# Kernel tuning notes

Measured on AMD Instinct MI355X. Metric: run time of the kernel, lower is better.

Reference implementation:

```python
import jax, jax.numpy as jnp
import numpy as np

N = 65536      # total nodes
B = 128        # graphs per batch
NPG = N // B   # nodes per graph (equal-size graphs)
IN = 128       # in_channels
H = 128        # hidden_channels
E = 1048576    # spatial edges
K = 8          # kNN neighbors
L = 3          # num_layers
EPS = 1e-5     # GraphNorm eps
SLOPE = 0.01   # leaky_relu default negative_slope


def setup_inputs() -> dict:
    key = jax.random.key(0)
    ks = jax.random.split(key, 16)
    x = jax.random.normal(ks[0], (N, IN), jnp.float32)
    edge_index = jax.random.randint(ks[1], (2, E), 0, N, dtype=jnp.int32)
    batch = jnp.repeat(jnp.arange(B, dtype=jnp.int32), NPG)
    s = 0.05
    inp = {
        'x': x, 'edge_index': edge_index, 'batch': batch,
        'emb_w': jax.random.normal(ks[2], (IN, H), jnp.float32) * s,
        'emb_b': jax.random.normal(ks[3], (H,), jnp.float32) * s,
        'conv_w': jax.random.normal(ks[4], (L - 1, H, H), jnp.float32) * s,
        'conv_b': jax.random.normal(ks[5], (L - 1, H), jnp.float32) * s,
        'fconv_w': jax.random.normal(ks[6], (L - 1, H, H), jnp.float32) * s,
        'fconv_b': jax.random.normal(ks[7], (L - 1, H), jnp.float32) * s,
        'norm_w': 1.0 + jax.random.normal(ks[8], (L - 1, H), jnp.float32) * s,
        'norm_b': jax.random.normal(ks[9], (L - 1, H), jnp.float32) * s,
        'norm_ms': 1.0 + jax.random.normal(ks[10], (L - 1, H), jnp.float32) * s,
        'fnorm_w': 1.0 + jax.random.normal(ks[11], (L - 1, H), jnp.float32) * s,
        'fnorm_b': jax.random.normal(ks[12], (L - 1, H), jnp.float32) * s,
        'fnorm_ms': 1.0 + jax.random.normal(ks[13], (L - 1, H), jnp.float32) * s,
    }
    return inp


def _segment_mean(v, seg, num):
    s = jax.ops.segment_sum(v, seg, num_segments=num)
    c = jax.ops.segment_sum(jnp.ones((v.shape[0], 1), v.dtype), seg, num_segments=num)
    return s / jnp.maximum(c, 1.0)


def _gcn_conv(h, src, dst, W, b):
    # GCNConv: h @ W, add self-loops, symmetric normalization, scatter-add.
    hw = h @ W
    deg = jax.ops.segment_sum(jnp.ones(src.shape[0], hw.dtype), dst, num_segments=N) + 1.0
    dinv = jax.lax.rsqrt(deg)
    msgs = (dinv[src] * dinv[dst])[:, None] * hw[src]
    agg = jnp.zeros_like(hw).at[dst].add(msgs)
    agg = agg + (dinv * dinv)[:, None] * hw  # self-loop contribution
    return agg + b


def _graph_norm(v, batch, w, bsh, ms):
    mean = _segment_mean(v, batch, B)                  # [B,H]
    out = v - mean[batch] * ms
    var = _segment_mean(out * out, batch, B)
    std = jnp.sqrt(var + EPS)
    return w * out / std[batch] + bsh


def _knn_graph_cosine(h):
    # per-graph cosine kNN (loop=False); equal-size graphs -> blocked [B,n,n] sim
    hb = h.reshape(B, NPG, H)
    nrm = jnp.linalg.norm(hb, axis=-1, keepdims=True)
    hn = hb / jnp.maximum(nrm, 1e-12)
    sim = jnp.einsum('bnd,bmd->bnm', hn, hn)
    sim = sim - 2.0 * jnp.eye(NPG, dtype=sim.dtype)    # exclude self-loops
    _, idx = jax.lax.top_k(sim, K)                     # [B,NPG,K] in-graph ids
    offs = (jnp.arange(B, dtype=idx.dtype) * NPG)[:, None, None]
    src = (idx + offs).reshape(-1).astype(jnp.int32)   # neighbors (sources)
    dst = jnp.repeat(jnp.arange(N, dtype=jnp.int32), K)
    return src, dst


def reference(x, edge_index, batch, emb_w, emb_b, conv_w, conv_b, fconv_w, fconv_b,
              norm_w, norm_b, norm_ms, fnorm_w, fnorm_b, fnorm_ms):
    h = x @ emb_w + emb_b
    fsrc, fdst = _knn_graph_cosine(h)
    src, dst = edge_index[0], edge_index[1]
    all_h = []
    for i in range(L - 1):
        h1 = _gcn_conv(h, src, dst, conv_w[i], conv_b[i])
        h1 = _graph_norm(h1, batch, norm_w[i], norm_b[i], norm_ms[i])
        h1 = jax.nn.leaky_relu(h1, SLOPE)              # dropout is identity (eval)
        f = _gcn_conv(h1, fsrc, fdst, fconv_w[i], fconv_b[i])
        f = _graph_norm(f, batch, fnorm_w[i], fnorm_b[i], fnorm_ms[i])
        f = jax.nn.leaky_relu(f, SLOPE)
        h = (h1 + f) * 0.5
        all_h.append(h)
    # faithful to original: indexes all_x[i-1] for i in range(num_layers)
    gf = jnp.zeros((B, H), h.dtype)
    for i in range(L):
        gf = gf + _segment_mean(all_h[i - 1], batch, B)
    return gf
```

## Files before the change

### kernel.cpp

```cpp
#include <hip/hip_runtime.h>

typedef unsigned short u16;
typedef unsigned int   u32;
typedef unsigned char  u8;
typedef __bf16 bf16x8 __attribute__((ext_vector_type(8)));
typedef unsigned short us8 __attribute__((ext_vector_type(8)));
typedef float f32x4 __attribute__((ext_vector_type(4)));

#define NN 65536
#define EE 1048576
#define NPGC 512
#define BGR 128
#define ESL 8
#define EMAX 32
#define FP8S 32.0f
#define FP8SI (1.0f/32.0f)

__device__ inline float bf2f(u16 b){ u32 u=((u32)b)<<16; float f; __builtin_memcpy(&f,&u,4); return f; }
__device__ inline u16 f2bf(float f){ u32 u; __builtin_memcpy(&u,&f,4); u32 r=(u+0x7FFFu+((u>>16)&1u))>>16; return (u16)r; }
__device__ inline u8 f2fp8(float f){
  int p = __builtin_amdgcn_cvt_pk_fp8_f32(f, f, 0, false);
  return (u8)(p & 0xFF);
}

struct PTab { const void* src[9]; int off[9]; };
__global__ __launch_bounds__(256) void prep_params(const float* __restrict__ emb_w,
    const float* __restrict__ conv_w, const float* __restrict__ fconv_w, u16* __restrict__ pwt,
    PTab tab, u16* __restrict__ pw)
{
  int i = blockIdx.x*256 + threadIdx.x;
  if (i < 5*16384) {
    int m = i >> 14, j = i & 16383;
    int n = j >> 7, k = j & 127;
    const float* src = (m == 0) ? emb_w : (m <= 2) ? conv_w + (m-1)*16384 : fconv_w + (m-3)*16384;
    pwt[i] = f2bf(src[k*128 + n]);
  } else {
    int s = i - 5*16384;
    if (s < 2176) {
      int t = 0;
      #pragma unroll
      for (int k = 1; k < 9; k++) if (s >= tab.off[k]) t = k;
      pw[s] = f2bf(((const float*)tab.src[t])[s - tab.off[t]]);
    }
  }
}

__global__ __launch_bounds__(256) void gemm_emb_bt(const float* __restrict__ X,
    const u16* __restrict__ BtE, const u16* __restrict__ bias, const u16* __restrict__ BtC,
    const float* __restrict__ dinvp, u16* __restrict__ Ch, float* __restrict__ rinv,
    u8* __restrict__ Chw)
{
  __shared__ __align__(16) u16 hs[64][136];
  const int tid = threadIdx.x;
  const int wave = tid >> 6, lane = tid & 63, q = lane >> 4, l15 = lane & 15;
  const long arow = (long)blockIdx.x*64 + wave*16 + l15;
  const float* Ap = X + arow*128;
  f32x4 acc[8] = {};
  #pragma unroll
  for (int ks = 0; ks < 4; ks++) {
    const int k0 = ks*32 + q*8;
    float4 u0 = *reinterpret_cast<const float4*>(Ap + k0);
    float4 u1 = *reinterpret_cast<const float4*>(Ap + k0 + 4);
    us8 a;
    a[0]=f2bf(u0.x); a[1]=f2bf(u0.y); a[2]=f2bf(u0.z); a[3]=f2bf(u0.w);
    a[4]=f2bf(u1.x); a[5]=f2bf(u1.y); a[6]=f2bf(u1.z); a[7]=f2bf(u1.w);
    bf16x8 af = __builtin_bit_cast(bf16x8, a);
    #pragma unroll
    for (int nt = 0; nt < 8; nt++) {
      bf16x8 bf = __builtin_bit_cast(bf16x8,
          *reinterpret_cast<const us8*>(BtE + (nt*16 + l15)*128 + k0));
      acc[nt] = __builtin_amdgcn_mfma_f32_16x16x32_bf16(af, bf, acc[nt], 0, 0, 0);
    }
  }
  const long orow0 = (long)blockIdx.x*64 + wave*16 + q*4;
  float bvt[8];
  #pragma unroll
  for (int nt = 0; nt < 8; nt++) bvt[nt] = bf2f(bias[nt*16 + l15]);
  #pragma unroll
  for (int r = 0; r < 4; r++) {
    float ss = 0.f;
    const int lrow = wave*16 + q*4 + r;
    #pragma unroll
    for (int nt = 0; nt < 8; nt++) {
      float hv = acc[nt][r] + bvt[nt];
      u16 hb = f2bf(hv);
      Ch[(orow0 + r)*128 + nt*16 + l15] = hb;
      hs[lrow][nt*16 + l15] = hb;
      ss += hv*hv;
    }
    #pragma unroll
    for (int m = 1; m < 16; m <<= 1) ss += __shfl_xor(ss, m, 64);
    if (l15 == 0) rinv[orow0 + r] = 1.0f / fmaxf(sqrtf(ss), 1e-12f);
  }
  __syncthreads();
  f32x4 acc2[8] = {};
  #pragma unroll
  for (int ks = 0; ks < 4; ks++) {
    const int k0 = ks*32 + q*8;
    bf16x8 af = __builtin_bit_cast(bf16x8,
        *reinterpret_cast<const us8*>(&hs[wave*16 + l15][k0]));
    #pragma unroll
    for (int nt = 0; nt < 8; nt++) {
      bf16x8 bf = __builtin_bit_cast(bf16x8,
          *reinterpret_cast<const us8*>(BtC + (nt*16 + l15)*128 + k0));
      acc2[nt] = __builtin_amdgcn_mfma_f32_16x16x32_bf16(af, bf, acc2[nt], 0, 0, 0);
    }
  }
  float scl[4];
  #pragma unroll
  for (int r = 0; r < 4; r++) scl[r] = dinvp[orow0 + r] * FP8S;
  #pragma unroll
  for (int nt = 0; nt < 8; nt++) {
    int col = nt*16 + l15;
    #pragma unroll
    for (int r = 0; r < 4; r++)
      Chw[(orow0 + r)*128 + col] = f2fp8(acc2[nt][r] * scl[r]);
  }
}

__global__ __launch_bounds__(256) void gemm_norm(const u16* __restrict__ h1raw,
    const u16* __restrict__ Bt, const float* __restrict__ ssum, const float* __restrict__ ssq,
    const u16* __restrict__ gw, const u16* __restrict__ gb, const u16* __restrict__ gms,
    u16* __restrict__ h1norm, u16* __restrict__ C)
{
  __shared__ float As[128], Bs[128];
  const int tid = threadIdx.x;
  const int gidx = blockIdx.x >> 3;
  if (tid < 128) {
    float mean = ssum[gidx*128 + tid] * (1.0f/512.0f);
    float e2   = ssq [gidx*128 + tid] * (1.0f/512.0f);
    float sub  = mean * bf2f(gms[tid]);
    float var  = e2 - 2.0f*sub*mean + sub*sub;
    float istd = rsqrtf(var + 1e-5f);
    float A = istd * bf2f(gw[tid]);
    As[tid] = A;
    Bs[tid] = bf2f(gb[tid]) - sub*A;
  }
  __syncthreads();
  const int wave = tid >> 6, lane = tid & 63, q = lane >> 4, l15 = lane & 15;
  const long arow = (long)blockIdx.x*64 + wave*16 + l15;
  const u16* Ap = h1raw + arow*128;
  f32x4 acc[8] = {};
  #pragma unroll
  for (int ks = 0; ks < 4; ks++) {
    const int k0 = ks*32 + q*8;
    us8 raw = *reinterpret_cast<const us8*>(Ap + k0);
    us8 af;
    #pragma unroll
    for (int j = 0; j < 8; j++) {
      float o = As[k0+j] * bf2f(raw[j]) + Bs[k0+j];
      o = (o >= 0.f) ? o : 0.01f * o;
      af[j] = f2bf(o);
    }
    *reinterpret_cast<us8*>(h1norm + arow*128 + k0) = af;
    bf16x8 afv = __builtin_bit_cast(bf16x8, af);
    #pragma unroll
    for (int nt = 0; nt < 8; nt++) {
      bf16x8 bf = __builtin_bit_cast(bf16x8,
          *reinterpret_cast<const us8*>(Bt + (nt*16 + l15)*128 + k0));
      acc[nt] = __builtin_amdgcn_mfma_f32_16x16x32_bf16(afv, bf, acc[nt], 0, 0, 0);
    }
  }
  const long orow0 = (long)blockIdx.x*64 + wave*16 + q*4;
  #pragma unroll
  for (int nt = 0; nt < 8; nt++) {
    int col = nt*16 + l15;
    #pragma unroll
    for (int r = 0; r < 4; r++)
      C[(orow0 + r)*128 + col] = f2bf(acc[nt][r]);
  }
}

__global__ __launch_bounds__(256) void gn_apply_gemm(const u16* __restrict__ fraw,
    const u16* __restrict__ h1n, const u16* __restrict__ Bt,
    const float* __restrict__ ssum, const float* __restrict__ ssq,
    const u16* __restrict__ gw, const u16* __restrict__ gb, const u16* __restrict__ gms,
    const float* __restrict__ dinvp, float* __restrict__ gf, u8* __restrict__ C)
{
  __shared__ float As[128], Bs[128];
  __shared__ float gpart[4][128];
  const int tid = threadIdx.x;
  const int gidx = blockIdx.x >> 3;
  if (tid < 128) {
    float mean = ssum[gidx*128 + tid] * (1.0f/512.0f);
    float e2   = ssq [gidx*128 + tid] * (1.0f/512.0f);
    float sub  = mean * bf2f(gms[tid]);
    float var  = e2 - 2.0f*sub*mean + sub*sub;
    float istd = rsqrtf(var + 1e-5f);
    float A = istd * bf2f(gw[tid]);
    As[tid] = A;
    Bs[tid] = bf2f(gb[tid]) - sub*A;
  }
  __syncthreads();
  const int wave = tid >> 6, lane = tid & 63, q = lane >> 4, l15 = lane & 15;
  const long arow = (long)blockIdx.x*64 + wave*16 + l15;
  const u16* Fp = fraw + arow*128;
  const u16* Hp = h1n  + arow*128;
  f32x4 acc[8] = {};
  float hv[4][8];
  #pragma unroll
  for (int ks = 0; ks < 4; ks++) {
    const int k0 = ks*32 + q*8;
    us8 fr = *reinterpret_cast<const us8*>(Fp + k0);
    us8 hr = *reinterpret_cast<const us8*>(Hp + k0);
    us8 af;
    #pragma unroll
    for (int j = 0; j < 8; j++) {
      float o = As[k0+j] * bf2f(fr[j]) + Bs[k0+j];
      o = (o >= 0.f) ? o : 0.01f * o;
      float h = 0.5f * (bf2f(hr[j]) + o);
      hv[ks][j] = h;
      af[j] = f2bf(h);
    }
    bf16x8 afv = __builtin_bit_cast(bf16x8, af);
    #pragma unroll
    for (int nt = 0; nt < 8; nt++) {
      bf16x8 bf = __builtin_bit_cast(bf16x8,
          *reinterpret_cast<const us8*>(Bt + (nt*16 + l15)*128 + k0));
      acc[nt] = __builtin_amdgcn_mfma_f32_16x16x32_bf16(afv, bf, acc[nt], 0, 0, 0);
    }
  }
  const long orow0 = (long)blockIdx.x*64 + wave*16 + q*4;
  float scl[4];
  #pragma unroll
  for (int r = 0; r < 4; r++) scl[r] = dinvp[orow0 + r] * FP8S;
  #pragma unroll
  for (int nt = 0; nt < 8; nt++) {
    int col = nt*16 + l15;
    #pragma unroll
    for (int r = 0; r < 4; r++)
      C[(orow0 + r)*128 + col] = f2fp8(acc[nt][r] * scl[r]);
  }
  #pragma unroll
  for (int ks = 0; ks < 4; ks++) {
    #pragma unroll
    for (int j = 0; j < 8; j++) {
      float v = hv[ks][j];
      v += __shfl_xor(v, 1, 64);
      v += __shfl_xor(v, 2, 64);
      v += __shfl_xor(v, 4, 64);
      v += __shfl_xor(v, 8, 64);
      if (l15 == 0) gpart[wave][ks*32 + q*8 + j] = v;
    }
  }
  __syncthreads();
  if (tid < 128) {
    float s = gpart[0][tid] + gpart[1][tid] + gpart[2][tid] + gpart[3][tid];
    atomicAdd(&gf[gidx*128 + tid], s * (1.0f/512.0f));
  }
}

__global__ void fill_ell(const int* __restrict__ srcp, const int* __restrict__ dstp,
    int* __restrict__ pos2, u16* __restrict__ ell){
  int base = (blockIdx.x*256 + threadIdx.x) * 4;
  int cls = blockIdx.x & 7;
  int4 dv = *reinterpret_cast<const int4*>(dstp + base);
  int4 sv = *reinterpret_cast<const int4*>(srcp + base);
  #pragma unroll
  for (int t = 0; t < 4; t++) {
    int d = ((&dv.x)[t]) & (NN-1);
    int p = atomicAdd(&pos2[cls*NN + d], 1);
    if (p < ESL) ell[((size_t)cls*NN + d)*ESL + p] = (u16)(((&sv.x)[t]) & (NN-1));
  }
}

__global__ __launch_bounds__(256) void repack_ell(const int* __restrict__ pos2,
    const u16* __restrict__ ell_cls, u16* __restrict__ elln, int* __restrict__ deg,
    float* __restrict__ dinv)
{
  int n = blockIdx.x*256 + threadIdx.x;
  u16* dst = elln + ((size_t)n << 5);
  int w = 0, tot = 0;
  #pragma unroll
  for (int c = 0; c < 8; c++) {
    int cnt = pos2[c*NN + n];
    tot += cnt;
    cnt = min(cnt, ESL);
    us8 iv = *reinterpret_cast<const us8*>(ell_cls + ((size_t)c*NN + n)*ESL);
    for (int t = 0; t < cnt; t++) { if (w < EMAX) dst[w] = iv[t]; w++; }
  }
  deg[n] = min(w, EMAX);
  dinv[n] = rsqrtf((float)tot + 1.0f);
}

__device__ inline u32 mkkey(float v, u32 col){
  u32 b; __builtin_memcpy(&b, &v, 4);
  b ^= (u32)(((int)b >> 31)) | 0x80000000u;
  return (b & 0xFFFFFE00u) | col;
}
#define TOP8_INS(tv, key) { \
  tv[0] = max(tv[0], (key)); \
  u32 lo_, hi_; \
  lo_ = min(tv[0],tv[1]); hi_ = max(tv[0],tv[1]); tv[0]=lo_; tv[1]=hi_; \
  lo_ = min(tv[1],tv[2]); hi_ = max(tv[1],tv[2]); tv[1]=lo_; tv[2]=hi_; \
  lo_ = min(tv[2],tv[3]); hi_ = max(tv[2],tv[3]); tv[2]=lo_; tv[3]=hi_; \
  lo_ = min(tv[3],tv[4]); hi_ = max(tv[3],tv[4]); tv[3]=lo_; tv[4]=hi_; \
  lo_ = min(tv[4],tv[5]); hi_ = max(tv[4],tv[5]); tv[4]=lo_; tv[5]=hi_; \
  lo_ = min(tv[5],tv[6]); hi_ = max(tv[5],tv[6]); tv[5]=lo_; tv[6]=hi_; \
  lo_ = min(tv[6],tv[7]); hi_ = max(tv[6],tv[7]); tv[6]=lo_; tv[7]=hi_; }

__global__ __launch_bounds__(256, 4) void knn_topk(const u16* __restrict__ h,
    const float* __restrict__ rinv, int* __restrict__ fsrc)
{
  __shared__ __align__(16) u16 Bb[64*136];
  __shared__ __align__(16) u32 simb[64*68];
  __shared__ float rb[64];
  const int tid = threadIdx.x;
  const int g = blockIdx.x & 127, tile = blockIdx.x >> 7;
  const int gbase = g * NPGC;
  const int abase = gbase + tile * 64;
  const int wave = tid >> 6, lane = tid & 63, q = lane >> 4, l15 = lane & 15;

  us8 afr[4];
  #pragma unroll
  for (int ks = 0; ks < 4; ks++)
    afr[ks] = *reinterpret_cast<const us8*>(h + (size_t)(abase + wave*16 + l15)*128 + ks*32 + q*8);

  const int r0 = tid >> 4, c80 = (tid & 15) * 8;
  us8 breg[4];
  #pragma unroll
  for (int it = 0; it < 4; it++)
    breg[it] = *reinterpret_cast<const us8*>(h + (size_t)(gbase + r0 + it*16)*128 + c80);
  float rbreg = (tid < 64) ? rinv[gbase + tid] : 0.f;

  const int srow = tid >> 2, ssub = tid & 3;
  u32 tv[8];
  #pragma unroll
  for (int t = 0; t < 8; t++) tv[t] = 0u;

  for (int ch = 0; ch < 8; ch++) {
    #pragma unroll
    for (int it = 0; it < 4; it++)
      *reinterpret_cast<us8*>(&Bb[(r0 + it*16)*136 + c80]) = breg[it];
    if (tid < 64) rb[tid] = rbreg;
    __syncthreads();
    if (ch < 7) {
      #pragma unroll
      for (int it = 0; it < 4; it++)
        breg[it] = *reinterpret_cast<const us8*>(h + (size_t)(gbase + (ch+1)*64 + r0 + it*16)*128 + c80);
      if (tid < 64) rbreg = rinv[gbase + (ch+1)*64 + tid];
    }
    f32x4 acc[4] = {};
    #pragma unroll
    for (int ks = 0; ks < 4; ks++) {
      int k0 = ks*32 + q*8;
      bf16x8 af = __builtin_bit_cast(bf16x8, afr[ks]);
      #pragma unroll
      for (int ct = 0; ct < 4; ct++) {
        bf16x8 bf = __builtin_bit_cast(bf16x8, *reinterpret_cast<const us8*>(&Bb[(ct*16 + l15)*136 + k0]));
        acc[ct] = __builtin_amdgcn_mfma_f32_16x16x32_bf16(af, bf, acc[ct], 0, 0, 0);
      }
    }
    #pragma unroll
    for (int ct = 0; ct < 4; ct++) {
      int lc = ct*16 + l15;
      float rbv = rb[lc];
      #pragma unroll
      for (int r = 0; r < 4; r++) {
        int lr = wave*16 + q*4 + r;
        u32 key = mkkey(acc[ct][r] * rbv, (u32)(ch*64 + lc));
        if (tile*64 + lr == ch*64 + lc) key = 0u;
        simb[lr*68 + lc] = key;
      }
    }
    __syncthreads();
    const u32* sp = &simb[srow*68 + ssub*16];
    #pragma unroll
    for (int u = 0; u < 4; u++) {
      uint4 kv = *reinterpret_cast<const uint4*>(sp + 4*u);
      TOP8_INS(tv, kv.x); TOP8_INS(tv, kv.y); TOP8_INS(tv, kv.z); TOP8_INS(tv, kv.w);
    }
    __syncthreads();
  }
  u32* candk = simb;
  #pragma unroll
  for (int t = 0; t < 8; t++) candk[srow*33 + ssub*8 + t] = tv[t];
  __syncthreads();
  if (tid < 64) {
    u32 bv[8];
    #pragma unroll
    for (int t = 0; t < 8; t++) bv[t] = 0u;
    for (int t = 0; t < 32; t++) {
      u32 key = candk[tid*33 + t];
      TOP8_INS(bv, key);
    }
    size_t node = abase + tid;
    #pragma unroll
    for (int k2 = 0; k2 < 8; k2++) fsrc[node*8 + k2] = gbase + (int)(bv[k2] & 511u);
  }
}

__device__ inline void acc4(u32 vv, bool on, float& a0, float& a1, float& a2, float& a3){
  float c0 = __builtin_amdgcn_cvt_f32_fp8((int)vv, 0);
  float c1 = __builtin_amdgcn_cvt_f32_fp8((int)vv, 1);
  float c2 = __builtin_amdgcn_cvt_f32_fp8((int)vv, 2);
  float c3 = __builtin_amdgcn_cvt_f32_fp8((int)vv, 3);
  a0 += on ? c0 : 0.f; a1 += on ? c1 : 0.f;
  a2 += on ? c2 : 0.f; a3 += on ? c3 : 0.f;
}
__global__ __launch_bounds__(256) void agg_spatial(const u32* __restrict__ hw32,
    const u16* __restrict__ elln, const int* __restrict__ deg, const float* __restrict__ dinv,
    const u16* __restrict__ bias, u16* __restrict__ outp,
    float* __restrict__ ssum, float* __restrict__ ssq)
{
  __shared__ f32x4 sred[4][64], qred[4][64];
  const int g = blockIdx.x & 127, sub = blockIdx.x >> 7;
  const int wave = threadIdx.x >> 6, lane = threadIdx.x & 63;
  const int half = lane >> 5, cl = lane & 31;
  const int nbase = g*NPGC + sub*32 + wave*8;
  float bv[4];
  #pragma unroll
  for (int k = 0; k < 4; k++) bv[k] = bf2f(bias[4*cl + k]);
  float sa0=0,sa1=0,sa2=0,sa3=0, qa0=0,qa1=0,qa2=0,qa3=0;
  for (int t = 0; t < 4; t++) {
    const int node = nbase + 2*t + half;
    const u16* row = elln + ((size_t)node << 5);
    const int d = deg[node];
    const int dmax = max(d, __shfl_xor(d, 32, 64));
    const float dnS = dinv[node] * FP8SI;
    const u32 sv = hw32[(size_t)node*32 + cl];
    float a0=0,a1=0,a2=0,a3=0;
    if (dmax > 0) {
      us8 iv0 = *reinterpret_cast<const us8*>(row);
      us8 iv1 = *reinterpret_cast<const us8*>(row + 8);
      u32 v[16];
      #pragma unroll
      for (int u = 0; u < 8; u++) v[u] = hw32[(size_t)iv0[u]*32 + cl];
      const bool two = (dmax > 8);
      if (two) {
        #pragma unroll
        for (int u = 0; u < 8; u++) v[8+u] = hw32[(size_t)iv1[u]*32 + cl];
      }
      #pragma unroll
      for (int u = 0; u < 8; u++) acc4(v[u], u < d, a0, a1, a2, a3);
      if (two) {
        #pragma unroll
        for (int u = 0; u < 8; u++) acc4(v[8+u], 8+u < d, a0, a1, a2, a3);
      }
    }
    if (dmax > 16) {
      us8 iv2 = *reinterpret_cast<const us8*>(row + 16);
      us8 iv3 = *reinterpret_cast<const us8*>(row + 24);
      u32 v[16];
      #pragma unroll
      for (int u = 0; u < 8; u++) v[u] = hw32[(size_t)iv2[u]*32 + cl];
      const bool four = (dmax > 24);
      if (four) {
        #pragma unroll
        for (int u = 0; u < 8; u++) v[8+u] = hw32[(size_t)iv3[u]*32 + cl];
      }
      #pragma unroll
      for (int u = 0; u < 8; u++) acc4(v[u], 16+u < d, a0, a1, a2, a3);
      if (four) {
        #pragma unroll
        for (int u = 0; u < 8; u++) acc4(v[8+u], 24+u < d, a0, a1, a2, a3);
      }
    }
    acc4(sv, true, a0, a1, a2, a3);
    float r0 = dnS*a0 + bv[0], r1 = dnS*a1 + bv[1];
    float r2 = dnS*a2 + bv[2], r3 = dnS*a3 + bv[3];
    u32* op = reinterpret_cast<u32*>(outp) + (size_t)node*64 + 2*cl;
    op[0] = (u32)f2bf(r0) | ((u32)f2bf(r1) << 16);
    op[1] = (u32)f2bf(r2) | ((u32)f2bf(r3) << 16);
    sa0 += r0; sa1 += r1; sa2 += r2; sa3 += r3;
    qa0 += r0*r0; qa1 += r1*r1; qa2 += r2*r2; qa3 += r3*r3;
  }
  sred[wave][lane] = (f32x4){sa0, sa1, sa2, sa3};
  qred[wave][lane] = (f32x4){qa0, qa1, qa2, qa3};
  __syncthreads();
  const int tid = threadIdx.x;
  if (tid < 128) {
    const int ccl = tid >> 2, k = tid & 3;
    float s = 0.f, qq = 0.f;
    #pragma unroll
    for (int w = 0; w < 4; w++) {
      s  += sred[w][ccl][k] + sred[w][32+ccl][k];
      qq += qred[w][ccl][k] + qred[w][32+ccl][k];
    }
    atomicAdd(&ssum[g*128 + tid], s);
    atomicAdd(&ssq [g*128 + tid], qq);
  }
}

__global__ __launch_bounds__(256) void agg_knn(const u16* __restrict__ hw, const int* __restrict__ fsrc,
    const u16* __restrict__ bias, u16* __restrict__ outp,
    float* __restrict__ ssum, float* __restrict__ ssq)
{
  __shared__ float4 red[4][64];
  const int g = blockIdx.x & 127, sub = blockIdx.x >> 7;
  const int wave = threadIdx.x >> 6, lane = threadIdx.x & 63;
  const int nbase = g*NPGC + sub*32 + wave*8;
  const u32* hwp = reinterpret_cast<const u32*>(hw);
  const float bv0 = bf2f(bias[2*lane]), bv1 = bf2f(bias[2*lane+1]);
  const float c = 1.0f / 9.0f;
  float s0 = 0.f, s1 = 0.f, q0 = 0.f, q1 = 0.f;
  for (int t = 0; t < 8; t++) {
    const int node = nbase + t;
    const int* fr = fsrc + (long)node*8;
    u32 sv = hwp[(long)node*64 + lane];
    float a0 = bf2f((u16)sv), a1 = bf2f((u16)(sv>>16));
    #pragma unroll
    for (int k2 = 0; k2 < 8; k2++) {
      int s = fr[k2] & (NN-1);
      u32 v = hwp[(long)s*64 + lane];
      a0 += bf2f((u16)v); a1 += bf2f((u16)(v>>16));
    }
    float r0 = a0*c + bv0;
    float r1 = a1*c + bv1;
    reinterpret_cast<u32*>(outp)[(long)node*64 + lane] = (u32)f2bf(r0) | ((u32)f2bf(r1) << 16);
    s0 += r0; s1 += r1; q0 += r0*r0; q1 += r1*r1;
  }
  red[wave][lane] = make_float4(s0, s1, q0, q1);
  __syncthreads();
  if (wave == 0) {
    float4 a = red[0][lane];
    #pragma unroll
    for (int k = 1; k < 4; k++) {
      float4 b = red[k][lane];
      a.x += b.x; a.y += b.y; a.z += b.z; a.w += b.w;
    }
    atomicAdd(&ssum[g*128 + 2*lane],     a.x);
    atomicAdd(&ssum[g*128 + 2*lane + 1], a.y);
    atomicAdd(&ssq [g*128 + 2*lane],     a.z);
    atomicAdd(&ssq [g*128 + 2*lane + 1], a.w);
  }
}

__global__ __launch_bounds__(1024) void gn_final(const u16* __restrict__ v, const u16* __restrict__ h1n,
    const float* __restrict__ ssum, const float* __restrict__ ssq,
    const u16* __restrict__ gw, const u16* __restrict__ gb, const u16* __restrict__ gms,
    const float* __restrict__ gf, float* __restrict__ outf)
{
  __shared__ float red[1024];
  const int tid = threadIdx.x;
  const int g = blockIdx.x >> 1, half = blockIdx.x & 1;
  const int cl = tid & 63, c = half*64 + cl;
  const int rsub = tid >> 6;
  const long base = (long)g * NPGC * 128;
  float mean = ssum[g*128 + c] * (1.0f/512.0f);
  float e2   = ssq [g*128 + c] * (1.0f/512.0f);
  float sub  = mean * bf2f(gms[c]);
  float var  = e2 - 2.0f*sub*mean + sub*sub;
  float istd = rsqrtf(var + 1e-5f);
  float A = istd * bf2f(gw[c]);
  float B = bf2f(gb[c]) - sub*A;
  float gsum = 0.f;
  for (int r = rsub; r < NPGC; r += 16) {
    long idx = base + (long)r*128 + c;
    float o = A * bf2f(v[idx]) + B;
    o = (o >= 0.f) ? o : 0.01f * o;
    o = 0.5f * (bf2f(h1n[idx]) + o);
    gsum += o;
  }
  red[tid] = gsum; __syncthreads();
  if (tid < 64) {
    float t = 0.f;
    for (int k = 0; k < 16; k++) t += red[cl + k*64];
    int oi = g*128 + half*64 + tid;
    outf[oi] = gf[oi] + 2.0f * t * (1.0f/512.0f);
  }
}

extern "C" void kernel_launch(void* const* d_in, const int* in_sizes, int n_in,
                              void* d_out, int out_size, void* d_ws, size_t ws_size,
                              hipStream_t stream)
{
  const float* x  = (const float*)d_in[0];
  const int*   ei = (const int*)d_in[1];

  char* p = (char*)d_ws;
  auto alloc = [&](size_t b){ void* r = (void*)p; p += ((b + 255) & ~(size_t)255); return r; };
  u16*   h_bf   = (u16*)  alloc((size_t)NN*128*2);
  u16*   f_bf   = (u16*)  alloc((size_t)NN*128*2);
  u16*   h1_bf  = (u16*)  alloc((size_t)NN*128*2);
  int*   fsrc   = (int*)  alloc((size_t)NN*8*4);
  u16*   elln   = (u16*)  alloc((size_t)NN*32*2);
  int*   deg    = (int*)  alloc((size_t)NN*4);
  float* dinv   = (float*)alloc((size_t)NN*4);
  float* rinv   = (float*)alloc((size_t)NN*4);
  int*   pos2   = (int*)  alloc((size_t)8*NN*4);
  float* gf     = (float*)alloc((size_t)BGR*128*4);
  float* stats  = (float*)alloc((size_t)8*BGR*128*4);
  u16*   pw     = (u16*)  alloc((size_t)2176*2);
  u16*   pwt    = (u16*)  alloc((size_t)5*16384*2);
  char*  shared = (char*) alloc((size_t)NN*128*2);
  u16*   ell_cls = (u16*)shared;
  u16*   hw_bf   = (u16*)shared;
  u8*    hw_f8   = (u8*) shared;

  const int O_EMBB=0, O_CONVB=128, O_FCONVB=384, O_NW=640, O_NB=896, O_NMS=1152,
            O_FNW=1408, O_FNB=1664, O_FNMS=1920;
  PTab tab;
  const int srcidx[9] = {4,6,8,9,10,11,12,13,14};
  const int offs[9]   = {O_EMBB,O_CONVB,O_FCONVB,O_NW,O_NB,O_NMS,O_FNW,O_FNB,O_FNMS};
  for (int t = 0; t < 9; t++) { tab.src[t] = d_in[srcidx[t]]; tab.off[t] = offs[t]; }

  const int* srcp = ei;
  const int* dstp = ei + EE;

  (void)hipMemsetAsync(pos2, 0, (size_t)8*NN*4 + (size_t)BGR*128*4 + (size_t)8*BGR*128*4, stream);

  prep_params<<<329, 256, 0, stream>>>((const float*)d_in[3], (const float*)d_in[5],
                                       (const float*)d_in[7], pwt, tab, pw);
  fill_ell<<<1024, 256, 0, stream>>>(srcp, dstp, pos2, ell_cls);
  repack_ell<<<256, 256, 0, stream>>>(pos2, ell_cls, elln, deg, dinv);
  gemm_emb_bt<<<1024, 256, 0, stream>>>(x, pwt + 0, pw + O_EMBB, pwt + 1*16384, dinv,
                                        h_bf, rinv, hw_f8);
  knn_topk<<<1024, 256, 0, stream>>>(h_bf, rinv, fsrc);

  float* ssS0 = stats + 0*BGR*128; float* sqS0 = stats + 1*BGR*128;
  float* ssF0 = stats + 2*BGR*128; float* sqF0 = stats + 3*BGR*128;
  float* ssS1 = stats + 4*BGR*128; float* sqS1 = stats + 5*BGR*128;
  float* ssF1 = stats + 6*BGR*128; float* sqF1 = stats + 7*BGR*128;

  agg_spatial<<<2048, 256, 0, stream>>>((const u32*)hw_f8, elln, deg, dinv, pw + O_CONVB,
                                        h1_bf, ssS0, sqS0);
  gemm_norm<<<1024, 256, 0, stream>>>(h1_bf, pwt + 3*16384, ssS0, sqS0,
                                      pw + O_NW, pw + O_NB, pw + O_NMS,
                                      h_bf , hw_bf);
  agg_knn<<<2048, 256, 0, stream>>>(hw_bf, fsrc, pw + O_FCONVB, f_bf, ssF0, sqF0);
  gn_apply_gemm<<<1024, 256, 0, stream>>>(f_bf, h_bf, pwt + 2*16384, ssF0, sqF0,
                                          pw + O_FNW, pw + O_FNB, pw + O_FNMS,
                                          dinv, gf, hw_f8);
  agg_spatial<<<2048, 256, 0, stream>>>((const u32*)hw_f8, elln, deg, dinv, pw + O_CONVB + 128,
                                        h1_bf, ssS1, sqS1);
  gemm_norm<<<1024, 256, 0, stream>>>(h1_bf, pwt + 4*16384, ssS1, sqS1,
                                      pw + O_NW + 128, pw + O_NB + 128, pw + O_NMS + 128,
                                      h_bf , hw_bf);
  agg_knn<<<2048, 256, 0, stream>>>(hw_bf, fsrc, pw + O_FCONVB + 128, f_bf, ssF1, sqF1);
  gn_final<<<256, 1024, 0, stream>>>(f_bf, h_bf, ssF1, sqF1,
                                     pw + O_FNW + 128, pw + O_FNB + 128, pw + O_FNMS + 128,
                                     gf, (float*)d_out);
}
```

Baseline: 413.3 us.

## Build ELL adjacency directly with destination-partitioned atomics, drop repack kernel

Replaces the two-pass ELL build (eight per-class 8-slot buckets followed by a repack kernel) with a single pass. Each block reads a chunk of edges and only inserts those whose destination falls in its partition, writing straight into the 32-slot per-node list. Degree and the rsqrt normalisation are now recomputed on the fly from the position counter in the consumer kernels. The aim is to remove the repack launch and the deg/dinv arrays; in exchange every edge is read by eight blocks, and edges are now lost only past 32 per node rather than past 8 per class.

```diff
diff --git a/kernel.cpp b/kernel.cpp
--- a/kernel.cpp
+++ b/kernel.cpp
@@ -11,7 +11,6 @@
 #define EE 1048576
 #define NPGC 512
 #define BGR 128
-#define ESL 8
 #define EMAX 32
 #define FP8S 32.0f
 #define FP8SI (1.0f/32.0f)
@@ -45,9 +44,31 @@
   }
 }
 
+__global__ __launch_bounds__(256) void fill_ell(const int* __restrict__ srcp,
+    const int* __restrict__ dstp, int* __restrict__ pos, u16* __restrict__ elln)
+{
+  const int part  = blockIdx.x & 7;
+  const int chunk = blockIdx.x >> 3;
+  const int tid = threadIdx.x;
+  #pragma unroll
+  for (int v = 0; v < 8; v++) {
+    const int e = chunk*8192 + (v*256 + tid)*4;
+    int4 dv = *reinterpret_cast<const int4*>(dstp + e);
+    int4 sv = *reinterpret_cast<const int4*>(srcp + e);
+    #pragma unroll
+    for (int t = 0; t < 4; t++) {
+      int d = ((&dv.x)[t]) & (NN-1);
+      if ((d >> 13) == part) {
+        int p = atomicAdd(&pos[d], 1);
+        if (p < EMAX) elln[((size_t)d << 5) + p] = (u16)(((&sv.x)[t]) & (NN-1));
+      }
+    }
+  }
+}
+
 __global__ __launch_bounds__(256) void gemm_emb_bt(const float* __restrict__ X,
     const u16* __restrict__ BtE, const u16* __restrict__ bias, const u16* __restrict__ BtC,
-    const float* __restrict__ dinvp, u16* __restrict__ Ch, float* __restrict__ rinv,
+    const int* __restrict__ pos, u16* __restrict__ Ch, float* __restrict__ rinv,
     u8* __restrict__ Chw)
 {
   __shared__ __align__(16) u16 hs[64][136];
@@ -108,7 +129,7 @@
   }
   float scl[4];
   #pragma unroll
-  for (int r = 0; r < 4; r++) scl[r] = dinvp[orow0 + r] * FP8S;
+  for (int r = 0; r < 4; r++) scl[r] = rsqrtf((float)pos[orow0 + r] + 1.0f) * FP8S;
   #pragma unroll
   for (int nt = 0; nt < 8; nt++) {
     int col = nt*16 + l15;
@@ -175,7 +196,7 @@
     const u16* __restrict__ h1n, const u16* __restrict__ Bt,
     const float* __restrict__ ssum, const float* __restrict__ ssq,
     const u16* __restrict__ gw, const u16* __restrict__ gb, const u16* __restrict__ gms,
-    const float* __restrict__ dinvp, float* __restrict__ gf, u8* __restrict__ C)
+    const int* __restrict__ pos, float* __restrict__ gf, u8* __restrict__ C)
 {
   __shared__ float As[128], Bs[128];
   __shared__ float gpart[4][128];
@@ -223,7 +244,7 @@
   const long orow0 = (long)blockIdx.x*64 + wave*16 + q*4;
   float scl[4];
   #pragma unroll
-  for (int r = 0; r < 4; r++) scl[r] = dinvp[orow0 + r] * FP8S;
+  for (int r = 0; r < 4; r++) scl[r] = rsqrtf((float)pos[orow0 + r] + 1.0f) * FP8S;
   #pragma unroll
   for (int nt = 0; nt < 8; nt++) {
     int col = nt*16 + l15;
@@ -248,39 +269,6 @@
     float s = gpart[0][tid] + gpart[1][tid] + gpart[2][tid] + gpart[3][tid];
     atomicAdd(&gf[gidx*128 + tid], s * (1.0f/512.0f));
   }
-}
-
-__global__ void fill_ell(const int* __restrict__ srcp, const int* __restrict__ dstp,
-    int* __restrict__ pos2, u16* __restrict__ ell){
-  int base = (blockIdx.x*256 + threadIdx.x) * 4;
-  int cls = blockIdx.x & 7;
-  int4 dv = *reinterpret_cast<const int4*>(dstp + base);
-  int4 sv = *reinterpret_cast<const int4*>(srcp + base);
-  #pragma unroll
-  for (int t = 0; t < 4; t++) {
-    int d = ((&dv.x)[t]) & (NN-1);
-    int p = atomicAdd(&pos2[cls*NN + d], 1);
-    if (p < ESL) ell[((size_t)cls*NN + d)*ESL + p] = (u16)(((&sv.x)[t]) & (NN-1));
-  }
-}
-
-__global__ __launch_bounds__(256) void repack_ell(const int* __restrict__ pos2,
-    const u16* __restrict__ ell_cls, u16* __restrict__ elln, int* __restrict__ deg,
-    float* __restrict__ dinv)
-{
-  int n = blockIdx.x*256 + threadIdx.x;
-  u16* dst = elln + ((size_t)n << 5);
-  int w = 0, tot = 0;
-  #pragma unroll
-  for (int c = 0; c < 8; c++) {
-    int cnt = pos2[c*NN + n];
-    tot += cnt;
-    cnt = min(cnt, ESL);
-    us8 iv = *reinterpret_cast<const us8*>(ell_cls + ((size_t)c*NN + n)*ESL);
-    for (int t = 0; t < cnt; t++) { if (w < EMAX) dst[w] = iv[t]; w++; }
-  }
-  deg[n] = min(w, EMAX);
-  dinv[n] = rsqrtf((float)tot + 1.0f);
 }
 
 __device__ inline u32 mkkey(float v, u32 col){
@@ -399,7 +387,7 @@
   a2 += on ? c2 : 0.f; a3 += on ? c3 : 0.f;
 }
 __global__ __launch_bounds__(256) void agg_spatial(const u32* __restrict__ hw32,
-    const u16* __restrict__ elln, const int* __restrict__ deg, const float* __restrict__ dinv,
+    const u16* __restrict__ elln, const int* __restrict__ pos,
     const u16* __restrict__ bias, u16* __restrict__ outp,
     float* __restrict__ ssum, float* __restrict__ ssq)
 {
@@ -415,9 +403,10 @@
   for (int t = 0; t < 4; t++) {
     const int node = nbase + 2*t + half;
     const u16* row = elln + ((size_t)node << 5);
-    const int d = deg[node];
+    const int tot = pos[node];
+    const int d = min(tot, EMAX);
     const int dmax = max(d, __shfl_xor(d, 32, 64));
-    const float dnS = dinv[node] * FP8SI;
+    const float dnS = rsqrtf((float)tot + 1.0f) * FP8SI;
     const u32 sv = hw32[(size_t)node*32 + cl];
     float a0=0,a1=0,a2=0,a3=0;
     if (dmax > 0) {
@@ -575,16 +564,13 @@
   u16*   h1_bf  = (u16*)  alloc((size_t)NN*128*2);
   int*   fsrc   = (int*)  alloc((size_t)NN*8*4);
   u16*   elln   = (u16*)  alloc((size_t)NN*32*2);
-  int*   deg    = (int*)  alloc((size_t)NN*4);
-  float* dinv   = (float*)alloc((size_t)NN*4);
   float* rinv   = (float*)alloc((size_t)NN*4);
-  int*   pos2   = (int*)  alloc((size_t)8*NN*4);
+  int*   pos    = (int*)  alloc((size_t)NN*4);
   float* gf     = (float*)alloc((size_t)BGR*128*4);
   float* stats  = (float*)alloc((size_t)8*BGR*128*4);
   u16*   pw     = (u16*)  alloc((size_t)2176*2);
   u16*   pwt    = (u16*)  alloc((size_t)5*16384*2);
   char*  shared = (char*) alloc((size_t)NN*128*2);
-  u16*   ell_cls = (u16*)shared;
   u16*   hw_bf   = (u16*)shared;
   u8*    hw_f8   = (u8*) shared;
 
@@ -598,13 +584,12 @@
   const int* srcp = ei;
   const int* dstp = ei + EE;
 
-  (void)hipMemsetAsync(pos2, 0, (size_t)8*NN*4 + (size_t)BGR*128*4 + (size_t)8*BGR*128*4, stream);
+  (void)hipMemsetAsync(pos, 0, (size_t)NN*4 + (size_t)BGR*128*4 + (size_t)8*BGR*128*4, stream);
 
   prep_params<<<329, 256, 0, stream>>>((const float*)d_in[3], (const float*)d_in[5],
                                        (const float*)d_in[7], pwt, tab, pw);
-  fill_ell<<<1024, 256, 0, stream>>>(srcp, dstp, pos2, ell_cls);
-  repack_ell<<<256, 256, 0, stream>>>(pos2, ell_cls, elln, deg, dinv);
-  gemm_emb_bt<<<1024, 256, 0, stream>>>(x, pwt + 0, pw + O_EMBB, pwt + 1*16384, dinv,
+  fill_ell<<<1024, 256, 0, stream>>>(srcp, dstp, pos, elln);
+  gemm_emb_bt<<<1024, 256, 0, stream>>>(x, pwt + 0, pw + O_EMBB, pwt + 1*16384, pos,
                                         h_bf, rinv, hw_f8);
   knn_topk<<<1024, 256, 0, stream>>>(h_bf, rinv, fsrc);
 
@@ -613,7 +598,7 @@
   float* ssS1 = stats + 4*BGR*128; float* sqS1 = stats + 5*BGR*128;
   float* ssF1 = stats + 6*BGR*128; float* sqF1 = stats + 7*BGR*128;
 
-  agg_spatial<<<2048, 256, 0, stream>>>((const u32*)hw_f8, elln, deg, dinv, pw + O_CONVB,
+  agg_spatial<<<2048, 256, 0, stream>>>((const u32*)hw_f8, elln, pos, pw + O_CONVB,
                                         h1_bf, ssS0, sqS0);
   gemm_norm<<<1024, 256, 0, stream>>>(h1_bf, pwt + 3*16384, ssS0, sqS0,
                                       pw + O_NW, pw + O_NB, pw + O_NMS,
@@ -621,8 +606,8 @@
   agg_knn<<<2048, 256, 0, stream>>>(hw_bf, fsrc, pw + O_FCONVB, f_bf, ssF0, sqF0);
   gn_apply_gemm<<<1024, 256, 0, stream>>>(f_bf, h_bf, pwt + 2*16384, ssF0, sqF0,
                                           pw + O_FNW, pw + O_FNB, pw + O_FNMS,
-                                          dinv, gf, hw_f8);
-  agg_spatial<<<2048, 256, 0, stream>>>((const u32*)hw_f8, elln, deg, dinv, pw + O_CONVB + 128,
+                                          pos, gf, hw_f8);
+  agg_spatial<<<2048, 256, 0, stream>>>((const u32*)hw_f8, elln, pos, pw + O_CONVB + 128,
                                         h1_bf, ssS1, sqS1);
   gemm_norm<<<1024, 256, 0, stream>>>(h1_bf, pwt + 4*16384, ssS1, sqS1,
                                       pw + O_NW + 128, pw + O_NB + 128, pw + O_NMS + 128,
```

New measurement: 404.0 us. 1.02x faster.
